# Kernel optimization log

Measured on AMD Instinct MI355X. Metric: run time of the kernel, lower is better.

Reference implementation:

```python
import jax, jax.numpy as jnp
import numpy as np

DIM, HEADS, DIM_HEAD = 1024, 16, 64
DIM_INNER = HEADS * DIM_HEAD  # 1024
SCALE = DIM_HEAD ** -0.5


def _rope(t):
    # t: [b, h, n, d]; interleaved-pair RoPE (lucidrains rotary-embedding-torch default)
    d = t.shape[-1]
    n = t.shape[-2]
    inv_freq = 1.0 / (10000.0 ** (jnp.arange(0, d, 2, dtype=jnp.float32) / d))
    angles = jnp.arange(n, dtype=jnp.float32)[:, None] * inv_freq[None, :]  # [n, d/2]
    cos, sin = jnp.cos(angles), jnp.sin(angles)
    t1, t2 = t[..., 0::2], t[..., 1::2]
    r1 = t1 * cos - t2 * sin
    r2 = t1 * sin + t2 * cos
    return jnp.stack([r1, r2], axis=-1).reshape(t.shape)


def setup_inputs() -> dict:
    key = jax.random.key(0)
    ks = jax.random.split(key, 8)
    b, n = 2, 2048
    inp = {
        "x": jax.random.normal(ks[0], (b, n, DIM), dtype=jnp.float32),
        "value_residual": jax.random.normal(ks[1], (b, HEADS, n, DIM_HEAD), dtype=jnp.float32),
        "gamma": jnp.ones((DIM,), dtype=jnp.float32),
        "w_qkv": jax.random.normal(ks[2], (DIM, 3 * DIM_INNER), dtype=jnp.float32) * (DIM ** -0.5),
        "w_mix": jax.random.normal(ks[3], (DIM, HEADS), dtype=jnp.float32) * (DIM ** -0.5),
        "b_mix": jnp.zeros((HEADS,), dtype=jnp.float32),
        "w_gates": jax.random.normal(ks[4], (DIM, HEADS), dtype=jnp.float32) * (DIM ** -0.5),
        "b_gates": jnp.zeros((HEADS,), dtype=jnp.float32),
        "w_out": jax.random.normal(ks[5], (DIM_INNER, DIM), dtype=jnp.float32) * (DIM_INNER ** -0.5),
    }
    return inp


def reference(x, value_residual, gamma, w_qkv, w_mix, b_mix, w_gates, b_gates, w_out):
    b, n, _ = x.shape
    # RMSNorm (lucidrains style: F.normalize * sqrt(dim) * gamma)
    norm = jnp.sqrt(jnp.sum(x * x, axis=-1, keepdims=True))
    xn = x / jnp.maximum(norm, 1e-12) * (DIM ** 0.5) * gamma

    qkv = xn @ w_qkv  # [b, n, 3*h*d]
    qkv = qkv.reshape(b, n, 3, HEADS, DIM_HEAD)
    q, k, v = [jnp.transpose(qkv[:, :, i], (0, 2, 1, 3)) for i in range(3)]  # [b,h,n,d]
    original_values = v

    # learned value-residual lerp
    mix = jax.nn.sigmoid(xn @ w_mix + b_mix)            # [b, n, h]
    mix = jnp.transpose(mix, (0, 2, 1))[..., None]       # [b, h, n, 1]
    v = v * (1.0 - mix) + value_residual * mix

    # rotary on q, k
    q = _rope(q)
    k = _rope(k)

    scores = jnp.einsum("bhid,bhjd->bhij", q, k) * SCALE
    attn = jax.nn.softmax(scores, axis=-1)
    out = jnp.einsum("bhij,bhjd->bhid", attn, v)         # [b, h, n, d]

    gates = jax.nn.sigmoid(xn @ w_gates + b_gates)       # [b, n, h]
    out = out * jnp.transpose(gates, (0, 2, 1))[..., None]

    out = jnp.transpose(out, (0, 2, 1, 3)).reshape(b, n, DIM_INNER)
    return out @ w_out, original_values
```

## Files before the change

### kernel.cpp

```cpp
#include <hip/hip_runtime.h>
#include <hip/hip_bf16.h>
#include <math.h>

#define DIMSZ 1024
#define HEADS 16
#define DHEAD 64
#define NSEQ  2048
#define BATCH 2
#define ROWS  (BATCH*NSEQ)
#define SCALE 0.125f
#define LOG2E 1.4426950408889634f

typedef __attribute__((ext_vector_type(8))) short short8;
typedef __attribute__((ext_vector_type(4))) float floatx4;
typedef __attribute__((ext_vector_type(16))) float floatx16;
typedef __attribute__((ext_vector_type(4))) unsigned uintx4;

#define MFMA16(a,b,c) __builtin_amdgcn_mfma_f32_16x16x32_bf16(a,b,c,0,0,0)
#define MFMA32(a,b,c) __builtin_amdgcn_mfma_f32_32x32x16_bf16(a,b,c,0,0,0)

__device__ __forceinline__ void gl2lds16(const void* g, void* l) {
    __builtin_amdgcn_global_load_lds(
        (const __attribute__((address_space(1))) unsigned int*)g,
        (__attribute__((address_space(3))) unsigned int*)l, 16, 0, 0);
}

__device__ __forceinline__ unsigned short bf16r(float a) {
    unsigned u = __float_as_uint(a);
    u += 0x7fff + ((u >> 16) & 1);
    return (unsigned short)(u >> 16);
}
__device__ __forceinline__ unsigned pack_bf16(float a, float b) {
    unsigned ua = __float_as_uint(a), ub = __float_as_uint(b);
    ua += 0x7fff + ((ua >> 16) & 1);
    ub += 0x7fff + ((ub >> 16) & 1);
    return (ua >> 16) | (ub & 0xffff0000u);
}
__device__ __forceinline__ float2 bf2f(unsigned u) {
    float2 r;
    r.x = __uint_as_float(u << 16);
    r.y = __uint_as_float(u & 0xffff0000u);
    return r;
}
__device__ __forceinline__ unsigned cvtpk(float lo, float hi) {
    unsigned r;
    asm("v_cvt_pk_bf16_f32 %0, %1, %2" : "=v"(r) : "v"(lo), "v"(hi));
    return r;
}
__device__ __forceinline__ void pl32swap(unsigned &a, unsigned &b) {
#if __has_builtin(__builtin_amdgcn_permlane32_swap)
    auto r = __builtin_amdgcn_permlane32_swap(a, b, false, false);
    a = (unsigned)r[0]; b = (unsigned)r[1];
#else
    asm volatile("v_permlane32_swap_b32 %0, %1" : "+v"(a), "+v"(b));
#endif
}
__device__ __forceinline__ float fexp2(float x) {
#if __has_builtin(__builtin_amdgcn_exp2f)
    return __builtin_amdgcn_exp2f(x);
#else
    return exp2f(x);
#endif
}
__device__ __forceinline__ float fsin_rev(float x) {
#if __has_builtin(__builtin_amdgcn_sinf)
    return __builtin_amdgcn_sinf(x);
#else
    return __sinf(x * 6.28318530717958647692f);
#endif
}
__device__ __forceinline__ float fcos_rev(float x) {
#if __has_builtin(__builtin_amdgcn_cosf)
    return __builtin_amdgcn_cosf(x);
#else
    return __cosf(x * 6.28318530717958647692f);
#endif
}

#define SWZ(row) (((row) & 7) ^ (((row) >> 3) & 1))

__global__ __launch_bounds__(256) void transpose_all_kernel(
    const float* __restrict__ w_qkv, const float* __restrict__ w_out,
    const float* __restrict__ w_mix, const float* __restrict__ w_gates,
    unsigned short* __restrict__ wqkvT, unsigned short* __restrict__ woutT,
    unsigned short* __restrict__ wmgT)
{
    __shared__ float t[32][33];
    const int tx = threadIdx.x & 31, tyy = threadIdx.x >> 5;
    const int bx = blockIdx.x;
    const int k0 = blockIdx.y * 32;
    if (bx < 128) {
        const float* src;
        unsigned short* dst;
        int N, n0;
        if (bx < 96) { src = w_qkv; dst = wqkvT; N = 3*DIMSZ; n0 = bx*32; }
        else         { src = w_out; dst = woutT; N = DIMSZ;   n0 = (bx-96)*32; }
        #pragma unroll
        for (int i = 0; i < 4; i++)
            t[tyy*4 + i][tx] = src[(size_t)(k0 + tyy*4 + i)*N + n0 + tx];
        __syncthreads();
        #pragma unroll
        for (int i = 0; i < 4; i++)
            dst[(size_t)(n0 + tyy*4 + i)*DIMSZ + k0 + tx] = bf16r(t[tx][tyy*4 + i]);
    } else {
        #pragma unroll
        for (int i = 0; i < 4; i++) {
            const int kk = k0 + tyy*4 + i;
            t[tyy*4 + i][tx] = (tx < 16) ? w_mix[kk*16 + tx]
                                         : w_gates[kk*16 + (tx - 16)];
        }
        __syncthreads();
        #pragma unroll
        for (int i = 0; i < 4; i++)
            wmgT[(size_t)(tyy*4 + i)*DIMSZ + k0 + tx] = bf16r(t[tx][tyy*4 + i]);
    }
}

__global__ __launch_bounds__(256) void rmsnorm_kernel(
    const float* __restrict__ x, const float* __restrict__ gamma,
    unsigned short* __restrict__ xnb)
{
    const int row = blockIdx.x;
    const int tid = threadIdx.x;
    __shared__ float wred[4];

    const float4 xv = ((const float4*)(x + (size_t)row * DIMSZ))[tid];
    float ss = xv.x*xv.x + xv.y*xv.y + xv.z*xv.z + xv.w*xv.w;
    #pragma unroll
    for (int off = 1; off < 64; off <<= 1) ss += __shfl_xor(ss, off);
    if ((tid & 63) == 0) wred[tid >> 6] = ss;
    __syncthreads();
    const float total = wred[0] + wred[1] + wred[2] + wred[3];
    const float inv = 32.0f / fmaxf(sqrtf(total), 1e-12f);
    const float4 gv = ((const float4*)gamma)[tid];
    uint2 pk;
    pk.x = pack_bf16(xv.x * inv * gv.x, xv.y * inv * gv.y);
    pk.y = pack_bf16(xv.z * inv * gv.z, xv.w * inv * gv.w);
    ((uint2*)(xnb + (size_t)row * DIMSZ))[tid] = pk;
}

__global__ __launch_bounds__(256) void mix_gates_mfma(
    const unsigned short* __restrict__ A, const unsigned short* __restrict__ WG,
    const float* __restrict__ b_mix, const float* __restrict__ b_gates,
    float* __restrict__ mixo, float* __restrict__ gateso)
{
    __shared__ short As[128*32];
    __shared__ short Bs[32*32];
    const int tid = threadIdx.x;
    const int wv = tid >> 6, lane = tid & 63;
    const int g = lane >> 4, c = lane & 15;
    const int bm = blockIdx.x * 128;

    floatx4 acc[2][2];
    #pragma unroll
    for (int mt = 0; mt < 2; mt++)
        #pragma unroll
        for (int nt = 0; nt < 2; nt++) acc[mt][nt] = (floatx4){0.f,0.f,0.f,0.f};

    for (int k0 = 0; k0 < DIMSZ; k0 += 32) {
        __syncthreads();
        #pragma unroll
        for (int r = 0; r < 2; r++) {
            const int ch = tid + 256*r;
            const int row = ch >> 2, cc = ch & 3;
            gl2lds16(A + (size_t)(bm + row)*DIMSZ + k0 + cc*8, (void*)(As + ch*8));
        }
        if (tid < 128)
            gl2lds16(WG + (size_t)(tid >> 2)*DIMSZ + k0 + (tid & 3)*8, (void*)(Bs + tid*8));
        __syncthreads();
        short8 af[2], bf[2];
        #pragma unroll
        for (int mt = 0; mt < 2; mt++) af[mt] = *(const short8*)(As + (wv*32 + mt*16 + c)*32 + g*8);
        #pragma unroll
        for (int nt = 0; nt < 2; nt++) bf[nt] = *(const short8*)(Bs + (nt*16 + c)*32 + g*8);
        #pragma unroll
        for (int mt = 0; mt < 2; mt++)
            #pragma unroll
            for (int nt = 0; nt < 2; nt++)
                acc[mt][nt] = MFMA16(af[mt], bf[nt], acc[mt][nt]);
    }
    const float bm_c = b_mix[c], bg_c = b_gates[c];
    #pragma unroll
    for (int mt = 0; mt < 2; mt++)
        #pragma unroll
        for (int r2 = 0; r2 < 4; r2++) {
            const int row = bm + wv*32 + mt*16 + g*4 + r2;
            const float lm = acc[mt][0][r2] + bm_c;
            const float lg = acc[mt][1][r2] + bg_c;
            mixo[(size_t)row*HEADS + c]   = 1.0f / (1.0f + fexp2(-lm * LOG2E));
            gateso[(size_t)row*HEADS + c] = 1.0f / (1.0f + fexp2(-lg * LOG2E));
        }
}

__device__ __forceinline__ void stage_qkv(
    const unsigned short* A, const unsigned short* BT,
    short* as, short* bs, int bm, int bn, int kk, int tid)
{
    #pragma unroll
    for (int r = 0; r < 2; r++) {
        const int ch = tid + 256*r;
        const int row = ch >> 2, j = ch & 3;
        gl2lds16(A  + (size_t)(bm + row)*DIMSZ + kk + j*8, (void*)(as + ch*8));
        gl2lds16(BT + (size_t)(bn + row)*DIMSZ + kk + j*8, (void*)(bs + ch*8));
    }
}

__global__ __launch_bounds__(256) void gemm_qkv_mfma(
    const unsigned short* __restrict__ A, const unsigned short* __restrict__ BT,
    unsigned short* __restrict__ qb, unsigned short* __restrict__ kb,
    float* __restrict__ vb)
{
    __shared__ short As[3][128*32];
    __shared__ short Bs[3][128*32];
    const int tid = threadIdx.x;
    const int wv = tid >> 6, lane = tid & 63;
    const int g = lane >> 4, c = lane & 15;
    const int wm = wv >> 1, wn = wv & 1;

    const int id = blockIdx.y * gridDim.x + blockIdx.x;
    const int xcd = id & 7, j = id >> 3;
    const int bnb = (xcd & 1)*12 + (j % 12);
    const int byb = (xcd >> 1)*8 + (j / 12);
    const int bm = byb * 128, bn = bnb * 128;

    floatx4 acc[4][4];
    #pragma unroll
    for (int mt = 0; mt < 4; mt++)
        #pragma unroll
        for (int nt = 0; nt < 4; nt++) acc[mt][nt] = (floatx4){0.f,0.f,0.f,0.f};

    stage_qkv(A, BT, &As[0][0], &Bs[0][0], bm, bn, 0,  tid);
    stage_qkv(A, BT, &As[1][0], &Bs[1][0], bm, bn, 32, tid);
    asm volatile("s_waitcnt vmcnt(4)" ::: "memory");
    __builtin_amdgcn_s_barrier();
    __builtin_amdgcn_sched_barrier(0);

    int cur = 0, nxt = 2;
    for (int i = 0; i < 32; i++) {
        const int k0 = i*32;
        if (i < 30)
            stage_qkv(A, BT, &As[nxt][0], &Bs[nxt][0], bm, bn, k0 + 64, tid);

        short8 af[4], bf[4];
        #pragma unroll
        for (int mt = 0; mt < 4; mt++) af[mt] = *(const short8*)(&As[cur][0] + (wm*64 + mt*16 + c)*32 + g*8);
        #pragma unroll
        for (int nt = 0; nt < 4; nt++) bf[nt] = *(const short8*)(&Bs[cur][0] + (wn*64 + nt*16 + c)*32 + g*8);
        __builtin_amdgcn_s_setprio(1);
        #pragma unroll
        for (int mt = 0; mt < 4; mt++)
            #pragma unroll
            for (int nt = 0; nt < 4; nt++)
                acc[mt][nt] = MFMA16(af[mt], bf[nt], acc[mt][nt]);
        __builtin_amdgcn_s_setprio(0);

        if (i < 31) {
            if (i < 30) asm volatile("s_waitcnt vmcnt(4)" ::: "memory");
            else        asm volatile("s_waitcnt vmcnt(0)" ::: "memory");
            __builtin_amdgcn_s_barrier();
            __builtin_amdgcn_sched_barrier(0);
        }
        cur = (cur == 2) ? 0 : cur + 1;
        nxt = (nxt == 2) ? 0 : nxt + 1;
    }
    __syncthreads();

    const int i3 = bn >> 10;
    const int nb = bn - (i3 << 10);
    if (i3 < 2) {
        unsigned short* dst = (i3 == 0) ? qb : kb;
        short* wbuf = &As[0][0] + wv*1152;
        const int rd_row = lane >> 2, seg = lane & 3;
        #pragma unroll
        for (int mt = 0; mt < 4; mt++) {
            #pragma unroll
            for (int nt = 0; nt < 4; nt++)
                #pragma unroll
                for (int r2 = 0; r2 < 4; r2++)
                    wbuf[(g*4 + r2)*72 + nt*16 + c] = (short)bf16r(acc[mt][nt][r2]);
            __builtin_amdgcn_s_waitcnt(0xc07f);
            const uint4 v0 = *(const uint4*)&wbuf[rd_row*72 + seg*16];
            const uint4 v1 = *(const uint4*)&wbuf[rd_row*72 + seg*16 + 8];
            const int row = bm + wm*64 + mt*16 + rd_row;
            const int col = nb + wn*64 + seg*16;
            const int hh = col >> 6, dd = col & 63;
            const int bb2 = row >> 11, pos = row & 2047;
            unsigned short* dp = dst + (((size_t)(bb2*HEADS + hh)*NSEQ) + pos)*DHEAD + dd;
            *(uint4*)dp = v0;
            *(uint4*)(dp + 8) = v1;
            __builtin_amdgcn_s_waitcnt(0xc07f);
        }
    } else {
        #pragma unroll
        for (int mt = 0; mt < 4; mt++)
            #pragma unroll
            for (int nt = 0; nt < 4; nt++)
                #pragma unroll
                for (int r2 = 0; r2 < 4; r2++) {
                    const int row = bm + wm*64 + mt*16 + g*4 + r2;
                    const int col = nb + wn*64 + nt*16 + c;
                    const int hh = col >> 6, dd = col & 63;
                    const int bb2 = row >> 11, pos = row & 2047;
                    vb[(((size_t)(bb2*HEADS + hh)*NSEQ) + pos)*DHEAD + dd] = acc[mt][nt][r2];
                }
    }
}

__global__ __launch_bounds__(256) void rope_blend_kernel2(
    unsigned short* __restrict__ q, unsigned short* __restrict__ k,
    const float* __restrict__ vorig, const float* __restrict__ vres,
    const float* __restrict__ mixb, unsigned short* __restrict__ vT)
{
    __shared__ unsigned short vt[64*72];
    const int tid = threadIdx.x;
    const int bh = blockIdx.y, bb = bh >> 4, h = bh & 15;
    const int p0 = blockIdx.x * 64;
    {
        const int pr = tid >> 2, d0 = (tid & 3) * 16;
        const int pos = p0 + pr;
        const size_t base = ((size_t)bh*NSEQ + pos)*DHEAD + d0;

        uint4 qr0 = *(uint4*)(q + base), qr1 = *(uint4*)(q + base + 8);
        uint4 kr0 = *(uint4*)(k + base), kr1 = *(uint4*)(k + base + 8);
        unsigned qw[8] = {qr0.x, qr0.y, qr0.z, qr0.w, qr1.x, qr1.y, qr1.z, qr1.w};
        unsigned kw[8] = {kr0.x, kr0.y, kr0.z, kr0.w, kr1.x, kr1.y, kr1.z, kr1.w};
        const float QSC = SCALE * LOG2E;
        const float posf = (float)pos;
        #pragma unroll
        for (int j = 0; j < 8; j++) {
            const float pf = (float)((d0 >> 1) + j);
            const float rev = posf * fexp2(-pf * 0.41524101186092029f
                                           - 2.6514961294723187f);
            const float rf = rev - floorf(rev);
            const float sn = fsin_rev(rf);
            const float cs = fcos_rev(rf);
            float2 qv = bf2f(qw[j]);
            float2 kv = bf2f(kw[j]);
            const float q1 = qv.x*cs - qv.y*sn, q2 = qv.x*sn + qv.y*cs;
            const float k1 = kv.x*cs - kv.y*sn, k2 = kv.x*sn + kv.y*cs;
            qw[j] = pack_bf16(q1*QSC, q2*QSC);
            kw[j] = pack_bf16(k1, k2);
        }
        *(uint4*)(q + base)     = *(uint4*)(qw + 0);
        *(uint4*)(q + base + 8) = *(uint4*)(qw + 4);
        *(uint4*)(k + base)     = *(uint4*)(kw + 0);
        *(uint4*)(k + base + 8) = *(uint4*)(kw + 4);

        float vv[16], vr[16];
        #pragma unroll
        for (int i = 0; i < 4; i++) {
            *(float4*)(vv + i*4) = *(const float4*)(vorig + base + i*4);
            *(float4*)(vr + i*4) = *(const float4*)(vres + base + i*4);
        }
        const float mx = mixb[((size_t)(bb*NSEQ + pos))*HEADS + h];
        #pragma unroll
        for (int j = 0; j < 8; j++) {
            const float b0 = vv[2*j]*(1.f-mx)   + vr[2*j]*mx;
            const float b1 = vv[2*j+1]*(1.f-mx) + vr[2*j+1]*mx;
            vt[pr*72 + d0 + 2*j]     = bf16r(b0);
            vt[pr*72 + d0 + 2*j + 1] = bf16r(b1);
        }
    }
    __syncthreads();
    {
        const int dd = tid >> 2, c0 = (tid & 3) * 16;
        unsigned o[8];
        #pragma unroll
        for (int j = 0; j < 8; j++) {
            const unsigned a  = vt[(c0 + 2*j)*72 + dd];
            const unsigned b2 = vt[(c0 + 2*j + 1)*72 + dd];
            o[j] = a | (b2 << 16);
        }
        unsigned short* dst = vT + ((size_t)bh*DHEAD + dd)*NSEQ + p0 + c0;
        *(uint4*)(dst)     = *(uint4*)(o + 0);
        *(uint4*)(dst + 8) = *(uint4*)(o + 4);
    }
}

__global__ __launch_bounds__(256, 4) void attn_mfma_kernel(
    const unsigned short* __restrict__ qg,
    const unsigned short* __restrict__ kg,
    const unsigned short* __restrict__ vT,
    unsigned short* __restrict__ Op0,
    unsigned short* __restrict__ Op1,
    float* __restrict__ lpart)
{
    __shared__ short Kt[2][64*64];
    __shared__ short Vt[2][64*64];

    const int tid = threadIdx.x;
    const int w = tid >> 6, lane = tid & 63;
    const int hi = lane >> 5, cq = lane & 31;

    int wg = blockIdx.y * gridDim.x + blockIdx.x;
    wg = (wg & 7) * 128 + (wg >> 3);
    const int q0 = (wg & 15) * 128;
    const int byy = wg >> 4;
    const int bh = byy >> 1, s = byy & 1;
    const int bb = bh >> 4, h = bh & 15;

    short8 qf[4];
    #pragma unroll
    for (int kd = 0; kd < 4; kd++)
        qf[kd] = *(const short8*)(qg + ((size_t)bh*NSEQ + q0 + w*32 + cq)*DHEAD + kd*16 + hi*8);

    short8 onesb;
    #pragma unroll
    for (int j = 0; j < 8; j++) onesb[j] = (short)0x3F80;

    floatx16 O0{}, O1{}, Ol{};

    const unsigned short* kbase = kg + (size_t)bh*NSEQ*DHEAD;
    const unsigned short* vbase = vT + (size_t)bh*DHEAD*NSEQ;

    {
        const int kt = s*16;
        #pragma unroll
        for (int r = 0; r < 2; r++) {
            const int ch = tid + 256*r;
            const int row = ch >> 3;
            const int u = (ch & 7) ^ SWZ(row);
            gl2lds16(kbase + (size_t)(kt*64 + row)*DHEAD + u*8, (void*)(&Kt[0][0] + ch*8));
            gl2lds16(vbase + (size_t)row*NSEQ + kt*64 + u*8,   (void*)(&Vt[0][0] + ch*8));
        }
    }
    __syncthreads();

    for (int i = 0; i < 16; i++) {
        const int cur = i & 1;
        const short* Ktc = &Kt[cur][0];
        const short* Vtc = &Vt[cur][0];

        if (i < 15) {
            const int kt = s*16 + i + 1;
            short* Ktn = &Kt[cur ^ 1][0];
            short* Vtn = &Vt[cur ^ 1][0];
            #pragma unroll
            for (int r = 0; r < 2; r++) {
                const int ch = tid + 256*r;
                const int row = ch >> 3;
                const int u = (ch & 7) ^ SWZ(row);
                gl2lds16(kbase + (size_t)(kt*64 + row)*DHEAD + u*8, (void*)(Ktn + ch*8));
                gl2lds16(vbase + (size_t)row*NSEQ + kt*64 + u*8,   (void*)(Vtn + ch*8));
            }
        }

        #pragma unroll
        for (int kt2 = 0; kt2 < 2; kt2++) {
            floatx16 accS{};
            const int rowk = kt2*32 + cq;
            __builtin_amdgcn_s_setprio(1);
            #pragma unroll
            for (int kd = 0; kd < 4; kd++) {
                short8 kf = *(const short8*)(Ktc + rowk*64 + (((kd*2 + hi) ^ SWZ(rowk)) * 8));
                accS = MFMA32(kf, qf[kd], accS);
            }
            __builtin_amdgcn_s_setprio(0);

            float p[16];
            #pragma unroll
            for (int r = 0; r < 16; r++) p[r] = fexp2(accS[r]);

            unsigned d0 = cvtpk(p[0],  p[1]);
            unsigned d1 = cvtpk(p[2],  p[3]);
            unsigned d2 = cvtpk(p[4],  p[5]);
            unsigned d3 = cvtpk(p[6],  p[7]);
            unsigned d4 = cvtpk(p[8],  p[9]);
            unsigned d5 = cvtpk(p[10], p[11]);
            unsigned d6 = cvtpk(p[12], p[13]);
            unsigned d7 = cvtpk(p[14], p[15]);
            pl32swap(d0, d2);
            pl32swap(d1, d3);
            pl32swap(d4, d6);
            pl32swap(d5, d7);
            const uintx4 t0 = {d0, d1, d2, d3};
            const uintx4 t1 = {d4, d5, d6, d7};
            const short8 pf0 = __builtin_bit_cast(short8, t0);
            const short8 pf1 = __builtin_bit_cast(short8, t1);

            __builtin_amdgcn_s_setprio(1);
            #pragma unroll
            for (int ks2 = 0; ks2 < 2; ks2++) {
                const short8 pf = ks2 ? pf1 : pf0;
                #pragma unroll
                for (int nt2 = 0; nt2 < 2; nt2++) {
                    const int rv = nt2*32 + cq;
                    short8 vf = *(const short8*)(Vtc + rv*64 + (((kt2*4 + ks2*2 + hi) ^ SWZ(rv)) * 8));
                    if (nt2 == 0) O0 = MFMA32(pf, vf, O0);
                    else          O1 = MFMA32(pf, vf, O1);
                }
                Ol = MFMA32(pf, onesb, Ol);
            }
            __builtin_amdgcn_s_setprio(0);
        }
        __syncthreads();
    }

    unsigned short* Op = s ? Op1 : Op0;
    if (cq == 0) {
        #pragma unroll
        for (int reg = 0; reg < 16; reg++) {
            const int qq = (reg & 3) + 8*(reg >> 2) + 4*hi;
            lpart[((size_t)s*ROWS + bb*NSEQ + q0 + w*32 + qq)*HEADS + h] = Ol[reg];
        }
    }
    #pragma unroll
    for (int reg = 0; reg < 16; reg++) {
        const int qq = (reg & 3) + 8*(reg >> 2) + 4*hi;
        const int rowg = q0 + w*32 + qq;
        unsigned short* op = Op + ((size_t)(bb*NSEQ + rowg))*DIMSZ + h*DHEAD + cq;
        op[0]  = bf16r(O0[reg]);
        op[32] = bf16r(O1[reg]);
    }
}

__global__ __launch_bounds__(256) void attn_combine_kernel(
    const unsigned short* __restrict__ Op1, const float* __restrict__ lpart,
    const float* __restrict__ gates, unsigned short* __restrict__ attnO)
{
    const int idx = blockIdx.x * 256 + threadIdx.x;
    const int row = idx >> 7;
    const int c8 = (idx & 127) * 8;
    const int h = c8 >> 6;
    const float l0 = lpart[(size_t)row*HEADS + h];
    const float l1 = lpart[((size_t)ROWS + row)*HEADS + h];
    const float gt = gates[(size_t)row*HEADS + h];
    const float sc = gt / (l0 + l1);
    const size_t base = (size_t)row*DIMSZ + c8;
    const uint4 a = *(const uint4*)(attnO + base);
    const uint4 b = *(const uint4*)(Op1 + base);
    const unsigned aw[4] = {a.x, a.y, a.z, a.w};
    const unsigned bw[4] = {b.x, b.y, b.z, b.w};
    unsigned o[4];
    #pragma unroll
    for (int j = 0; j < 4; j++) {
        const float2 fa = bf2f(aw[j]);
        const float2 fb = bf2f(bw[j]);
        o[j] = pack_bf16((fa.x + fb.x)*sc, (fa.y + fb.y)*sc);
    }
    *(uint4*)(attnO + base) = *(uint4*)o;
}

__device__ __forceinline__ void stage_out(
    const unsigned short* A, const unsigned short* BT,
    short* as, short* bs, int bm, int bn, int kk, int tid)
{
    #pragma unroll
    for (int r = 0; r < 2; r++) {
        const int ch = tid + 256*r;
        const int row = ch >> 2, j = ch & 3;
        gl2lds16(A + (size_t)(bm + row)*DIMSZ + kk + j*8, (void*)(as + ch*8));
    }
    gl2lds16(BT + (size_t)(bn + (tid >> 2))*DIMSZ + kk + (tid & 3)*8, (void*)(bs + tid*8));
}

__global__ __launch_bounds__(256) void gemm_out_mfma(
    const unsigned short* __restrict__ A, const unsigned short* __restrict__ BT,
    float* __restrict__ out0)
{
    __shared__ short As[3][128*32];
    __shared__ short Bs[3][64*32];
    const int tid = threadIdx.x;
    const int wv = tid >> 6, lane = tid & 63;
    const int g = lane >> 4, c = lane & 15;
    const int wm = wv >> 1, wn = wv & 1;

    const int id = blockIdx.y * gridDim.x + blockIdx.x;
    const int xcd = id & 7, j = id >> 3;
    const int bnb = j & 15, byb = xcd*4 + (j >> 4);
    const int bm = byb * 128, bn = bnb * 64;

    floatx4 acc[4][2];
    #pragma unroll
    for (int mt = 0; mt < 4; mt++)
        #pragma unroll
        for (int nt = 0; nt < 2; nt++) acc[mt][nt] = (floatx4){0.f,0.f,0.f,0.f};

    stage_out(A, BT, &As[0][0], &Bs[0][0], bm, bn, 0,  tid);
    stage_out(A, BT, &As[1][0], &Bs[1][0], bm, bn, 32, tid);
    asm volatile("s_waitcnt vmcnt(3)" ::: "memory");
    __builtin_amdgcn_s_barrier();
    __builtin_amdgcn_sched_barrier(0);

    int cur = 0, nxt = 2;
    for (int i = 0; i < 32; i++) {
        const int k0 = i*32;
        if (i < 30)
            stage_out(A, BT, &As[nxt][0], &Bs[nxt][0], bm, bn, k0 + 64, tid);

        short8 af[4], bf[2];
        #pragma unroll
        for (int mt = 0; mt < 4; mt++) af[mt] = *(const short8*)(&As[cur][0] + (wm*64 + mt*16 + c)*32 + g*8);
        #pragma unroll
        for (int nt = 0; nt < 2; nt++) bf[nt] = *(const short8*)(&Bs[cur][0] + (wn*32 + nt*16 + c)*32 + g*8);
        __builtin_amdgcn_s_setprio(1);
        #pragma unroll
        for (int mt = 0; mt < 4; mt++)
            #pragma unroll
            for (int nt = 0; nt < 2; nt++)
                acc[mt][nt] = MFMA16(af[mt], bf[nt], acc[mt][nt]);
        __builtin_amdgcn_s_setprio(0);

        if (i < 31) {
            if (i < 30) asm volatile("s_waitcnt vmcnt(3)" ::: "memory");
            else        asm volatile("s_waitcnt vmcnt(0)" ::: "memory");
            __builtin_amdgcn_s_barrier();
            __builtin_amdgcn_sched_barrier(0);
        }
        cur = (cur == 2) ? 0 : cur + 1;
        nxt = (nxt == 2) ? 0 : nxt + 1;
    }

    #pragma unroll
    for (int mt = 0; mt < 4; mt++)
        #pragma unroll
        for (int nt = 0; nt < 2; nt++)
            #pragma unroll
            for (int r2 = 0; r2 < 4; r2++) {
                const int row = bm + wm*64 + mt*16 + g*4 + r2;
                const int col = bn + wn*32 + nt*16 + c;
                out0[(size_t)row*DIMSZ + col] = acc[mt][nt][r2];
            }
}

extern "C" void kernel_launch(void* const* d_in, const int* in_sizes, int n_in,
                              void* d_out, int out_size, void* d_ws, size_t ws_size,
                              hipStream_t stream) {
    const float* x       = (const float*)d_in[0];
    const float* vres    = (const float*)d_in[1];
    const float* gamma   = (const float*)d_in[2];
    const float* w_qkv   = (const float*)d_in[3];
    const float* w_mix   = (const float*)d_in[4];
    const float* b_mix   = (const float*)d_in[5];
    const float* w_gates = (const float*)d_in[6];
    const float* b_gates = (const float*)d_in[7];
    const float* w_out   = (const float*)d_in[8];

    float* out0 = (float*)d_out;
    float* out1 = out0 + (size_t)ROWS * DIMSZ;

    char* ws = (char*)d_ws;
    unsigned short* xnb   = (unsigned short*)(ws);
    unsigned short* wqkvT = (unsigned short*)(ws + (8u<<20));
    unsigned short* woutT = (unsigned short*)(ws + (14u<<20));
    unsigned short* qb2   = (unsigned short*)(ws + (16u<<20));
    unsigned short* kb2   = (unsigned short*)(ws + (24u<<20));
    unsigned short* vT    = (unsigned short*)(ws + (32u<<20));
    unsigned short* attnO = (unsigned short*)(ws + (40u<<20));
    float*          mixb  = (float*)(ws + (48u<<20));
    float*          gatesb= (float*)(ws + (48u<<20) + 262144);
    unsigned short* wmgT  = (unsigned short*)(ws + (49u<<20));
    unsigned short* Op1   = (unsigned short*)(ws + (50u<<20));
    float*          lpart = (float*)(ws + (58u<<20));

    transpose_all_kernel<<<dim3(129, DIMSZ/32), 256, 0, stream>>>(
        w_qkv, w_out, w_mix, w_gates, wqkvT, woutT, wmgT);

    rmsnorm_kernel<<<ROWS, 256, 0, stream>>>(x, gamma, xnb);

    mix_gates_mfma<<<ROWS/128, 256, 0, stream>>>(
        xnb, wmgT, b_mix, b_gates, mixb, gatesb);

    gemm_qkv_mfma<<<dim3(3*DIMSZ/128, ROWS/128), 256, 0, stream>>>(
        xnb, wqkvT, qb2, kb2, out1);

    rope_blend_kernel2<<<dim3(NSEQ/64, BATCH*HEADS), 256, 0, stream>>>(
        qb2, kb2, out1, vres, mixb, vT);

    attn_mfma_kernel<<<dim3(NSEQ/128, BATCH*HEADS*2), 256, 0, stream>>>(
        qb2, kb2, vT, attnO, Op1, lpart);

    attn_combine_kernel<<<ROWS*DIMSZ/8/256, 256, 0, stream>>>(
        Op1, lpart, gatesb, attnO);

    gemm_out_mfma<<<dim3(DIMSZ/64, ROWS/128), 256, 0, stream>>>(
        attnO, woutT, out0);
}
```

Before: 233.7 us.

## Fuse RoPE into QKV GEMM epilogue via cos/sin table; compute row sums without MFMA

Builds a per-position cos/sin table in an extra block column of the transpose kernel. The QKV GEMM epilogue now applies RoPE and the q scaling before storing, so the blend kernel no longer re-reads and re-writes q and k. In attention, both QK^T MFMAs are issued up front. The softmax denominator is summed in registers with a cross-lane shuffle instead of an extra MFMA against a ones vector. In exchange, the GEMM epilogue gains table loads and rotation ALU work, and the precomputed table costs some extra memory traffic.

```diff
diff --git a/kernel.cpp b/kernel.cpp
--- a/kernel.cpp
+++ b/kernel.cpp
@@ -83,7 +83,7 @@
     const float* __restrict__ w_qkv, const float* __restrict__ w_out,
     const float* __restrict__ w_mix, const float* __restrict__ w_gates,
     unsigned short* __restrict__ wqkvT, unsigned short* __restrict__ woutT,
-    unsigned short* __restrict__ wmgT)
+    unsigned short* __restrict__ wmgT, float* __restrict__ rtab)
 {
     __shared__ float t[32][33];
     const int tx = threadIdx.x & 31, tyy = threadIdx.x >> 5;
@@ -102,7 +102,7 @@
         #pragma unroll
         for (int i = 0; i < 4; i++)
             dst[(size_t)(n0 + tyy*4 + i)*DIMSZ + k0 + tx] = bf16r(t[tx][tyy*4 + i]);
-    } else {
+    } else if (bx == 128) {
         #pragma unroll
         for (int i = 0; i < 4; i++) {
             const int kk = k0 + tyy*4 + i;
@@ -113,6 +113,21 @@
         #pragma unroll
         for (int i = 0; i < 4; i++)
             wmgT[(size_t)(tyy*4 + i)*DIMSZ + k0 + tx] = bf16r(t[tx][tyy*4 + i]);
+    } else {
+        const int pos = blockIdx.y*64 + (threadIdx.x >> 2);
+        const int f0 = (threadIdx.x & 3) * 8;
+        float2* dst = (float2*)rtab + (size_t)pos*32 + f0;
+        #pragma unroll
+        for (int tt = 0; tt < 8; tt++) {
+            const float pf = (float)(f0 + tt);
+            const float rev = (float)pos * fexp2(-pf * 0.41524101186092029f
+                                                 - 2.6514961294723187f);
+            const float rf = rev - floorf(rev);
+            float2 cs;
+            cs.x = fcos_rev(rf);
+            cs.y = fsin_rev(rf);
+            dst[tt] = cs;
+        }
     }
 }
 
@@ -207,6 +222,7 @@
 
 __global__ __launch_bounds__(256) void gemm_qkv_mfma(
     const unsigned short* __restrict__ A, const unsigned short* __restrict__ BT,
+    const float* __restrict__ rtab,
     unsigned short* __restrict__ qb, unsigned short* __restrict__ kb,
     float* __restrict__ vb)
 {
@@ -269,6 +285,7 @@
     const int nb = bn - (i3 << 10);
     if (i3 < 2) {
         unsigned short* dst = (i3 == 0) ? qb : kb;
+        const float fac = (i3 == 0) ? (SCALE * LOG2E) : 1.0f;
         short* wbuf = &As[0][0] + wv*1152;
         const int rd_row = lane >> 2, seg = lane & 3;
         #pragma unroll
@@ -285,9 +302,19 @@
             const int col = nb + wn*64 + seg*16;
             const int hh = col >> 6, dd = col & 63;
             const int bb2 = row >> 11, pos = row & 2047;
+            const float2* tp = (const float2*)rtab + (size_t)pos*32 + seg*8;
+            unsigned wv_[8] = {v0.x, v0.y, v0.z, v0.w, v1.x, v1.y, v1.z, v1.w};
+            #pragma unroll
+            for (int t = 0; t < 8; t++) {
+                const float2 cssn = tp[t];
+                const float2 pq = bf2f(wv_[t]);
+                const float r1 = (pq.x*cssn.x - pq.y*cssn.y) * fac;
+                const float r2 = (pq.x*cssn.y + pq.y*cssn.x) * fac;
+                wv_[t] = pack_bf16(r1, r2);
+            }
             unsigned short* dp = dst + (((size_t)(bb2*HEADS + hh)*NSEQ) + pos)*DHEAD + dd;
-            *(uint4*)dp = v0;
-            *(uint4*)(dp + 8) = v1;
+            *(uint4*)dp = (uint4){wv_[0], wv_[1], wv_[2], wv_[3]};
+            *(uint4*)(dp + 8) = (uint4){wv_[4], wv_[5], wv_[6], wv_[7]};
             __builtin_amdgcn_s_waitcnt(0xc07f);
         }
     } else {
@@ -306,8 +333,7 @@
     }
 }
 
-__global__ __launch_bounds__(256) void rope_blend_kernel2(
-    unsigned short* __restrict__ q, unsigned short* __restrict__ k,
+__global__ __launch_bounds__(256) void v_blend_kernel(
     const float* __restrict__ vorig, const float* __restrict__ vres,
     const float* __restrict__ mixb, unsigned short* __restrict__ vT)
 {
@@ -320,32 +346,6 @@
         const int pos = p0 + pr;
         const size_t base = ((size_t)bh*NSEQ + pos)*DHEAD + d0;
 
-        uint4 qr0 = *(uint4*)(q + base), qr1 = *(uint4*)(q + base + 8);
-        uint4 kr0 = *(uint4*)(k + base), kr1 = *(uint4*)(k + base + 8);
-        unsigned qw[8] = {qr0.x, qr0.y, qr0.z, qr0.w, qr1.x, qr1.y, qr1.z, qr1.w};
-        unsigned kw[8] = {kr0.x, kr0.y, kr0.z, kr0.w, kr1.x, kr1.y, kr1.z, kr1.w};
-        const float QSC = SCALE * LOG2E;
-        const float posf = (float)pos;
-        #pragma unroll
-        for (int j = 0; j < 8; j++) {
-            const float pf = (float)((d0 >> 1) + j);
-            const float rev = posf * fexp2(-pf * 0.41524101186092029f
-                                           - 2.6514961294723187f);
-            const float rf = rev - floorf(rev);
-            const float sn = fsin_rev(rf);
-            const float cs = fcos_rev(rf);
-            float2 qv = bf2f(qw[j]);
-            float2 kv = bf2f(kw[j]);
-            const float q1 = qv.x*cs - qv.y*sn, q2 = qv.x*sn + qv.y*cs;
-            const float k1 = kv.x*cs - kv.y*sn, k2 = kv.x*sn + kv.y*cs;
-            qw[j] = pack_bf16(q1*QSC, q2*QSC);
-            kw[j] = pack_bf16(k1, k2);
-        }
-        *(uint4*)(q + base)     = *(uint4*)(qw + 0);
-        *(uint4*)(q + base + 8) = *(uint4*)(qw + 4);
-        *(uint4*)(k + base)     = *(uint4*)(kw + 0);
-        *(uint4*)(k + base + 8) = *(uint4*)(kw + 4);
-
         float vv[16], vr[16];
         #pragma unroll
         for (int i = 0; i < 4; i++) {
@@ -404,11 +404,8 @@
     for (int kd = 0; kd < 4; kd++)
         qf[kd] = *(const short8*)(qg + ((size_t)bh*NSEQ + q0 + w*32 + cq)*DHEAD + kd*16 + hi*8);
 
-    short8 onesb;
-    #pragma unroll
-    for (int j = 0; j < 8; j++) onesb[j] = (short)0x3F80;
-
-    floatx16 O0{}, O1{}, Ol{};
+    floatx16 O0{}, O1{};
+    float lsum = 0.f;
 
     const unsigned short* kbase = kg + (size_t)bh*NSEQ*DHEAD;
     const unsigned short* vbase = vT + (size_t)bh*DHEAD*NSEQ;
@@ -445,21 +442,30 @@
             }
         }
 
+        floatx16 accS0{}, accS1{};
+        __builtin_amdgcn_s_setprio(1);
+        #pragma unroll
+        for (int kd = 0; kd < 4; kd++) {
+            const int r0 = cq, r1 = 32 + cq;
+            short8 kf0 = *(const short8*)(Ktc + r0*64 + (((kd*2 + hi) ^ SWZ(r0)) * 8));
+            short8 kf1 = *(const short8*)(Ktc + r1*64 + (((kd*2 + hi) ^ SWZ(r1)) * 8));
+            accS0 = MFMA32(kf0, qf[kd], accS0);
+            accS1 = MFMA32(kf1, qf[kd], accS1);
+        }
+        __builtin_amdgcn_s_setprio(0);
+
         #pragma unroll
         for (int kt2 = 0; kt2 < 2; kt2++) {
-            floatx16 accS{};
-            const int rowk = kt2*32 + cq;
-            __builtin_amdgcn_s_setprio(1);
-            #pragma unroll
-            for (int kd = 0; kd < 4; kd++) {
-                short8 kf = *(const short8*)(Ktc + rowk*64 + (((kd*2 + hi) ^ SWZ(rowk)) * 8));
-                accS = MFMA32(kf, qf[kd], accS);
-            }
-            __builtin_amdgcn_s_setprio(0);
+            const floatx16 accS = kt2 ? accS1 : accS0;
 
             float p[16];
             #pragma unroll
             for (int r = 0; r < 16; r++) p[r] = fexp2(accS[r]);
+            const float a1 = (p[0]+p[1]) + (p[2]+p[3]);
+            const float a2 = (p[4]+p[5]) + (p[6]+p[7]);
+            const float a3 = (p[8]+p[9]) + (p[10]+p[11]);
+            const float a4 = (p[12]+p[13]) + (p[14]+p[15]);
+            lsum += (a1+a2) + (a3+a4);
 
             unsigned d0 = cvtpk(p[0],  p[1]);
             unsigned d1 = cvtpk(p[2],  p[3]);
@@ -489,7 +495,6 @@
                     if (nt2 == 0) O0 = MFMA32(pf, vf, O0);
                     else          O1 = MFMA32(pf, vf, O1);
                 }
-                Ol = MFMA32(pf, onesb, Ol);
             }
             __builtin_amdgcn_s_setprio(0);
         }
@@ -497,13 +502,9 @@
     }
 
     unsigned short* Op = s ? Op1 : Op0;
-    if (cq == 0) {
-        #pragma unroll
-        for (int reg = 0; reg < 16; reg++) {
-            const int qq = (reg & 3) + 8*(reg >> 2) + 4*hi;
-            lpart[((size_t)s*ROWS + bb*NSEQ + q0 + w*32 + qq)*HEADS + h] = Ol[reg];
-        }
-    }
+    float l = lsum + __shfl_xor(lsum, 32);
+    if (hi == 0)
+        lpart[((size_t)s*ROWS + bb*NSEQ + q0 + w*32 + cq)*HEADS + h] = l;
     #pragma unroll
     for (int reg = 0; reg < 16; reg++) {
         const int qq = (reg & 3) + 8*(reg >> 2) + 4*hi;
@@ -652,9 +653,10 @@
     unsigned short* wmgT  = (unsigned short*)(ws + (49u<<20));
     unsigned short* Op1   = (unsigned short*)(ws + (50u<<20));
     float*          lpart = (float*)(ws + (58u<<20));
-
-    transpose_all_kernel<<<dim3(129, DIMSZ/32), 256, 0, stream>>>(
-        w_qkv, w_out, w_mix, w_gates, wqkvT, woutT, wmgT);
+    float*          rtab  = (float*)(ws + (59u<<20));
+
+    transpose_all_kernel<<<dim3(130, DIMSZ/32), 256, 0, stream>>>(
+        w_qkv, w_out, w_mix, w_gates, wqkvT, woutT, wmgT, rtab);
 
     rmsnorm_kernel<<<ROWS, 256, 0, stream>>>(x, gamma, xnb);
 
@@ -662,10 +664,10 @@
         xnb, wmgT, b_mix, b_gates, mixb, gatesb);
 
     gemm_qkv_mfma<<<dim3(3*DIMSZ/128, ROWS/128), 256, 0, stream>>>(
-        xnb, wqkvT, qb2, kb2, out1);
-
-    rope_blend_kernel2<<<dim3(NSEQ/64, BATCH*HEADS), 256, 0, stream>>>(
-        qb2, kb2, out1, vres, mixb, vT);
+        xnb, wqkvT, rtab, qb2, kb2, out1);
+
+    v_blend_kernel<<<dim3(NSEQ/64, BATCH*HEADS), 256, 0, stream>>>(
+        out1, vres, mixb, vT);
 
     attn_mfma_kernel<<<dim3(NSEQ/128, BATCH*HEADS*2), 256, 0, stream>>>(
         qb2, kb2, vT, attnO, Op1, lpart);
```

New measurement: 253.7 us. 8.6% more time.
